# Kernel tuning notes

Hardware: AMD Instinct MI355X
Metric: run time of the kernel (lower is better)

## Reference

```python
import jax, jax.numpy as jnp
import numpy as np

B, T, D, H, C = 2048, 512, 1, 50, 2  # batch, seq_len, input_size, hidden_size, num_classes


def setup_inputs() -> dict:
    key = jax.random.key(0)
    ks = jax.random.split(key, 11)
    k = 1.0 / np.sqrt(H)  # torch default init bound
    u = lambda kk, shape: jax.random.uniform(kk, shape, jnp.float32, -k, k)
    return {
        "x": jax.random.normal(ks[0], (B, T, D), jnp.float32),
        "W_ih0": u(ks[1], (4 * H, D)),
        "W_hh0": u(ks[2], (4 * H, H)),
        "b_ih0": u(ks[3], (4 * H,)),
        "b_hh0": u(ks[4], (4 * H,)),
        "W_ih1": u(ks[5], (4 * H, H)),
        "W_hh1": u(ks[6], (4 * H, H)),
        "b_ih1": u(ks[7], (4 * H,)),
        "b_hh1": u(ks[8], (4 * H,)),
        "W_fc": u(ks[9], (C, H)),
        "b_fc": u(ks[10], (C,)),
    }


def _lstm_layer(x, Wih, Whh, bih, bhh):
    # x: [B, T, Din] -> hidden sequence [B, T, H]. PyTorch gate order: i, f, g, o.
    Bn = x.shape[0]
    Hn = Whh.shape[1]
    # precompute input contribution for all timesteps (one big GEMM)
    xg = jnp.einsum('btd,gd->btg', x, Wih) + bih + bhh  # [B, T, 4H]

    def step(carry, xg_t):
        h, c = carry
        g = xg_t + h @ Whh.T  # [B, 4H]
        i, f, gg, o = jnp.split(g, 4, axis=-1)
        i = jax.nn.sigmoid(i)
        f = jax.nn.sigmoid(f)
        gg = jnp.tanh(gg)
        o = jax.nn.sigmoid(o)
        c = f * c + i * gg
        h = o * jnp.tanh(c)
        return (h, c), h

    h0 = jnp.zeros((Bn, Hn), x.dtype)
    c0 = jnp.zeros((Bn, Hn), x.dtype)
    (_, _), hs = jax.lax.scan(step, (h0, c0), jnp.swapaxes(xg, 0, 1))  # hs: [T, B, H]
    return jnp.swapaxes(hs, 0, 1)


def reference(x, W_ih0, W_hh0, b_ih0, b_hh0, W_ih1, W_hh1, b_ih1, b_hh1, W_fc, b_fc):
    h1 = _lstm_layer(x, W_ih0, W_hh0, b_ih0, b_hh0)
    h2 = _lstm_layer(h1, W_ih1, W_hh1, b_ih1, b_hh1)
    # out[:, -1, :] @ W_fc.T + b_fc  (last-timestep hidden -> classifier)
    return h2[:, -1, :] @ W_fc.T + b_fc
```

## Files before the change

kernel.cpp:

```cpp
#include <hip/hip_runtime.h>

#define T_SEQ 512
#define HID   50
#define NB    8
#define BLK   832

typedef float v4f  __attribute__((ext_vector_type(4)));
typedef _Float16 f16;
typedef f16  f16x8 __attribute__((ext_vector_type(8)));


__device__ __forceinline__ f16x8 ldA0(const float* __restrict__ Whh0,
                                      const float* __restrict__ Wih0,
                                      const float* __restrict__ bih0,
                                      const float* __restrict__ bhh0,
                                      int m, int kb) {
    const int u = m >> 2, g = m & 3;
    f16x8 v;
    #pragma unroll
    for (int j = 0; j < 8; ++j) {
        const int k = kb + j;
        float f = 0.f;
        if (u < HID) {
            const int rho = g * HID + u;
            if (k < HID)      f = Whh0[rho * HID + k];
            else if (k == 62) f = Wih0[rho];
            else if (k == 63) f = bih0[rho] + bhh0[rho];
        }
        v[j] = (f16)f;
    }
    return v;
}

__device__ __forceinline__ f16x8 ldA1a(const float* __restrict__ Wih1,
                                       const float* __restrict__ bih1,
                                       const float* __restrict__ bhh1,
                                       int m, int kb) {
    const int u = m >> 2, g = m & 3;
    f16x8 v;
    #pragma unroll
    for (int j = 0; j < 8; ++j) {
        const int k = kb + j;
        float f = 0.f;
        if (u < HID) {
            const int rho = g * HID + u;
            if (k < HID)      f = Wih1[rho * HID + k];
            else if (k == 63) f = bih1[rho] + bhh1[rho];
        }
        v[j] = (f16)f;
    }
    return v;
}

__device__ __forceinline__ f16x8 ldA1b(const float* __restrict__ Whh1,
                                       int m, int kb) {
    const int u = m >> 2, g = m & 3;
    f16x8 v;
    #pragma unroll
    for (int j = 0; j < 8; ++j) {
        const int k = kb + j;
        float f = 0.f;
        if (u < HID && k < HID) f = Whh1[(g * HID + u) * HID + k];
        v[j] = (f16)f;
    }
    return v;
}

#define MFMA16(A, B, C) __builtin_amdgcn_mfma_f32_16x16x32_f16((A), (B), (C), 0, 0, 0)

__device__ __forceinline__ float lstm_epi(const v4f CC, float& cs) {
    const float e1 = __expf(-CC.x);
    const float e2 = __expf(-CC.y);
    const float e3 = __expf(-2.f * CC.z);
    const float e4 = __expf(-CC.w);
    const float d1 = 1.f + e1, d2 = 1.f + e2, d3 = 1.f + e3, d4 = 1.f + e4;
    const float p2 = d1 * d2, p3 = p2 * d3, p4 = p3 * d4;
    const float i4 = __builtin_amdgcn_rcpf(p4);
    const float go = i4 * p3;
    const float i3 = i4 * d4;
    const float r3 = i3 * p2;
    const float i2 = i3 * d3;
    const float gf = i2 * d1;
    const float gi = i2 * d2;
    const float gg = fmaf(2.f, r3, -1.f);
    cs = fmaf(gf, cs, gi * gg);
    const float th = fmaf(2.f, __builtin_amdgcn_rcpf(1.f + __expf(-2.f * cs)), -1.f);
    return go * th;
}

__global__ __launch_bounds__(BLK, 1)
void lstm2_mfma(const float* __restrict__ x,
                const float* __restrict__ Wih0,
                const float* __restrict__ Whh0,
                const float* __restrict__ bih0,
                const float* __restrict__ bhh0,
                const float* __restrict__ Wih1,
                const float* __restrict__ Whh1,
                const float* __restrict__ bih1,
                const float* __restrict__ bhh1,
                const float* __restrict__ Wfc,
                const float* __restrict__ bfc,
                float* __restrict__ out)
{
    __shared__ __align__(16) f16 BPH [8 * 64 * 8];
    __shared__ f16   xs16[NB][T_SEQ];
    __shared__ float hfin[HID][NB];

    const int tid  = threadIdx.x;
    const int w    = tid >> 6;
    const int lane = tid & 63;
    const int n16  = lane & 15;
    const int quad = lane >> 4;
    const int bb0  = blockIdx.x * NB;

    const float* xg = x + (long)bb0 * T_SEQ;

    for (int i = tid; i < 8 * 64 * 8; i += BLK) BPH[i] = (f16)0.f;
    for (int i = tid; i < NB * T_SEQ; i += BLK) {
        const int n = i >> 9, tt = i & (T_SEQ - 1);
        xs16[n][tt] = (f16)xg[n * T_SEQ + tt];
    }

    const int m   = w * 16 + n16;
    const int kb0 = quad * 8, kb1 = 32 + quad * 8;
    const f16x8 a0 = ldA0(Whh0, Wih0, bih0, bhh0, m, kb0);
    const f16x8 a1 = ldA0(Whh0, Wih0, bih0, bhh0, m, kb1);
    const f16x8 v0 = ldA1a(Wih1, bih1, bhh1, m, kb0);
    const f16x8 v1 = ldA1a(Wih1, bih1, bhh1, m, kb1);
    const f16x8 v2 = ldA1b(Whh1, m, kb0);
    const f16x8 v3 = ldA1b(Whh1, m, kb1);

    __syncthreads();
    if (tid < NB) {
        BPH[(1 * 64 + 48 + tid) * 8 + 7] = (f16)1.f;
        BPH[(1 * 64 + 56 + tid) * 8 + 7] = (f16)1.f;
        BPH[(3 * 64 + 48 + tid) * 8 + 7] = (f16)1.f;
        BPH[(3 * 64 + 56 + tid) * 8 + 7] = (f16)1.f;
        BPH[(3 * 64 + 48 + tid) * 8 + 6] = xs16[tid][0];
        BPH[(3 * 64 + 56 + tid) * 8 + 6] = xs16[tid][0];
    }
    __syncthreads();

    const int  u_    = w * 4 + quad;
    const bool isl0  = (n16 < 8);
    const bool valid = (u_ < HID);
    const int  wbase = (((u_ & 31) >> 3) * 16 + (n16 & 7)) * 8 + (u_ & 7) + (u_ >> 5) * 512;
    f16* const pwOdd  = &BPH[wbase + (isl0 ? 2 : 4) * 512];
    f16* const pwEven = &BPH[wbase + (isl0 ? 0 : 6) * 512];
    float cs = 0.f;
    const f16x8* BPF = (const f16x8*)BPH;
    const v4f CZ = {0.f, 0.f, 0.f, 0.f};

    {
        const f16x8 B0 = BPF[2 * 64 + lane];
        const f16x8 B1 = BPF[3 * 64 + lane];
        v4f D = MFMA16(a0, B0, CZ);  D = MFMA16(a1, B1, D);
        const float cs_sav = cs;
        const float hh = lstm_epi(D, cs);
        if (!isl0) cs = cs_sav;
        if (valid && isl0) { const f16 hv = (f16)hh; pwEven[0] = hv; pwEven[64] = hv; }
        if (w == 0 && lane < NB) {
            const f16 xv = xs16[lane][1];
            BPH[(1 * 64 + 48 + lane) * 8 + 6] = xv;
            BPH[(1 * 64 + 56 + lane) * 8 + 6] = xv;
        }
        __syncthreads();
    }

#define STEP(TA, TB, PW, XT, XS, DOX) {                                       \
        const f16x8 B0 = BPF[(TA)     * 64 + lane];                           \
        const f16x8 B1 = BPF[(TA + 1) * 64 + lane];                           \
        const f16x8 B2 = BPF[(TB)     * 64 + lane];                           \
        const f16x8 B3 = BPF[(TB + 1) * 64 + lane];                           \
        v4f D = MFMA16(a0, B0, CZ);  D = MFMA16(a1, B1, D);                   \
        v4f E = MFMA16(v0, B0, CZ);  E = MFMA16(v1, B1, E);                   \
        E = MFMA16(v2, B2, E);       E = MFMA16(v3, B3, E);                   \
        v4f CC;                                                               \
        CC.x = isl0 ? D.x : E.x;  CC.y = isl0 ? D.y : E.y;                    \
        CC.z = isl0 ? D.z : E.z;  CC.w = isl0 ? D.w : E.w;                    \
        const float hh = lstm_epi(CC, cs);                                    \
        if (valid) { const f16 hv = (f16)hh; (PW)[0] = hv; (PW)[64] = hv; }   \
        if ((DOX) && w == 0 && lane < NB) {                                   \
            const f16 xv = xs16[lane][(XS)];                                  \
            BPH[((XT) * 64 + 48 + lane) * 8 + 6] = xv;                        \
            BPH[((XT) * 64 + 56 + lane) * 8 + 6] = xv;                        \
        }                                                                     \
        __syncthreads(); }

    #pragma clang loop unroll(disable)
    for (int s = 1; s < 511; s += 2) {
        STEP(0, 6, pwOdd,  3, s + 1, true)
        STEP(2, 4, pwEven, 1, s + 2, true)
    }
    STEP(0, 6, pwOdd, 3, 0, false)

    {
        const f16x8 B0 = BPF[2 * 64 + lane];
        const f16x8 B1 = BPF[3 * 64 + lane];
        const f16x8 B2 = BPF[4 * 64 + lane];
        const f16x8 B3 = BPF[5 * 64 + lane];
        v4f E = MFMA16(v0, B0, CZ);  E = MFMA16(v1, B1, E);
        E = MFMA16(v2, B2, E);       E = MFMA16(v3, B3, E);
        const float hh = lstm_epi(E, cs);
        if (!isl0 && valid) hfin[u_][n16 & 7] = hh;
        __syncthreads();
    }

    if (tid < NB * 2) {
        const int nn = tid >> 1, c = tid & 1;
        float acc = bfc[c];
        #pragma unroll
        for (int u = 0; u < HID; ++u)
            acc = fmaf(Wfc[c * HID + u], hfin[u][nn], acc);
        out[(bb0 + nn) * 2 + c] = acc;
    }
}

extern "C" void kernel_launch(void* const* d_in, const int* in_sizes, int n_in,
                              void* d_out, int out_size, void* d_ws, size_t ws_size,
                              hipStream_t stream) {
    const float* x    = (const float*)d_in[0];
    const float* Wih0 = (const float*)d_in[1];
    const float* Whh0 = (const float*)d_in[2];
    const float* bih0 = (const float*)d_in[3];
    const float* bhh0 = (const float*)d_in[4];
    const float* Wih1 = (const float*)d_in[5];
    const float* Whh1 = (const float*)d_in[6];
    const float* bih1 = (const float*)d_in[7];
    const float* bhh1 = (const float*)d_in[8];
    const float* Wfc  = (const float*)d_in[9];
    const float* bfc  = (const float*)d_in[10];
    float* out = (float*)d_out;

    const int B = in_sizes[0] / T_SEQ;
    const int grid = B / NB;

    hipLaunchKernelGGL(lstm2_mfma, dim3(grid), dim3(BLK), 0, stream,
                       x, Wih0, Whh0, bih0, bhh0, Wih1, Whh1, bih1, bhh1,
                       Wfc, bfc, out);
}
```

Baseline: 327.3 us.

## Halve batch per block, double MFMA tiles per wave, fold log2e into weights

Each block now handles 4 sequences instead of 8 with 7 waves instead of 13. Each wave computes two 16-row gate tiles, and lanes pick their results from the two tiles so the 16 MFMA columns are used more fully. Launch bounds now allow up to 4 blocks per CU, with the aim of more concurrent blocks overlapping the per-step barriers and LDS latency. The log2(e) scaling, doubled for the g gate, is folded into the fp16 weights so the epilogue uses exp2 directly. The cost is twice the MFMA work per wave per step, more registers per thread, and slightly different fp16 rounding of the scaled weights.

```diff
diff --git a/kernel.cpp b/kernel.cpp
--- a/kernel.cpp
+++ b/kernel.cpp
@@ -2,13 +2,23 @@
 
 #define T_SEQ 512
 #define HID   50
-#define NB    8
-#define BLK   832
+#define NB    4
+#define BLK   448
 
 typedef float v4f  __attribute__((ext_vector_type(4)));
 typedef _Float16 f16;
 typedef f16  f16x8 __attribute__((ext_vector_type(8)));
 
+
+#define LOG2E 1.44269504f
+
+__device__ __forceinline__ float exp2g(float x) {
+#if __has_builtin(__builtin_amdgcn_exp2f)
+    return __builtin_amdgcn_exp2f(x);
+#else
+    return __builtin_exp2f(x);
+#endif
+}
 
 __device__ __forceinline__ f16x8 ldA0(const float* __restrict__ Whh0,
                                       const float* __restrict__ Wih0,
@@ -16,6 +26,7 @@
                                       const float* __restrict__ bhh0,
                                       int m, int kb) {
     const int u = m >> 2, g = m & 3;
+    const float sc = (g == 2) ? (2.f * LOG2E) : LOG2E;
     f16x8 v;
     #pragma unroll
     for (int j = 0; j < 8; ++j) {
@@ -27,7 +38,7 @@
             else if (k == 62) f = Wih0[rho];
             else if (k == 63) f = bih0[rho] + bhh0[rho];
         }
-        v[j] = (f16)f;
+        v[j] = (f16)(f * sc);
     }
     return v;
 }
@@ -37,6 +48,7 @@
                                        const float* __restrict__ bhh1,
                                        int m, int kb) {
     const int u = m >> 2, g = m & 3;
+    const float sc = (g == 2) ? (2.f * LOG2E) : LOG2E;
     f16x8 v;
     #pragma unroll
     for (int j = 0; j < 8; ++j) {
@@ -47,7 +59,7 @@
             if (k < HID)      f = Wih1[rho * HID + k];
             else if (k == 63) f = bih1[rho] + bhh1[rho];
         }
-        v[j] = (f16)f;
+        v[j] = (f16)(f * sc);
     }
     return v;
 }
@@ -55,13 +67,14 @@
 __device__ __forceinline__ f16x8 ldA1b(const float* __restrict__ Whh1,
                                        int m, int kb) {
     const int u = m >> 2, g = m & 3;
+    const float sc = (g == 2) ? (2.f * LOG2E) : LOG2E;
     f16x8 v;
     #pragma unroll
     for (int j = 0; j < 8; ++j) {
         const int k = kb + j;
         float f = 0.f;
         if (u < HID && k < HID) f = Whh1[(g * HID + u) * HID + k];
-        v[j] = (f16)f;
+        v[j] = (f16)(f * sc);
     }
     return v;
 }
@@ -69,10 +82,10 @@
 #define MFMA16(A, B, C) __builtin_amdgcn_mfma_f32_16x16x32_f16((A), (B), (C), 0, 0, 0)
 
 __device__ __forceinline__ float lstm_epi(const v4f CC, float& cs) {
-    const float e1 = __expf(-CC.x);
-    const float e2 = __expf(-CC.y);
-    const float e3 = __expf(-2.f * CC.z);
-    const float e4 = __expf(-CC.w);
+    const float e1 = exp2g(-CC.x);
+    const float e2 = exp2g(-CC.y);
+    const float e3 = exp2g(-CC.z);
+    const float e4 = exp2g(-CC.w);
     const float d1 = 1.f + e1, d2 = 1.f + e2, d3 = 1.f + e3, d4 = 1.f + e4;
     const float p2 = d1 * d2, p3 = p2 * d3, p4 = p3 * d4;
     const float i4 = __builtin_amdgcn_rcpf(p4);
@@ -84,11 +97,11 @@
     const float gi = i2 * d2;
     const float gg = fmaf(2.f, r3, -1.f);
     cs = fmaf(gf, cs, gi * gg);
-    const float th = fmaf(2.f, __builtin_amdgcn_rcpf(1.f + __expf(-2.f * cs)), -1.f);
+    const float th = fmaf(2.f, __builtin_amdgcn_rcpf(1.f + exp2g(-2.88539008f * cs)), -1.f);
     return go * th;
 }
 
-__global__ __launch_bounds__(BLK, 1)
+__global__ __launch_bounds__(BLK, 4)
 void lstm2_mfma(const float* __restrict__ x,
                 const float* __restrict__ Wih0,
                 const float* __restrict__ Whh0,
@@ -121,30 +134,37 @@
         xs16[n][tt] = (f16)xg[n * T_SEQ + tt];
     }
 
-    const int m   = w * 16 + n16;
+    const int mA  = (2 * w)     * 16 + n16;
+    const int mB  = (2 * w + 1) * 16 + n16;
     const int kb0 = quad * 8, kb1 = 32 + quad * 8;
-    const f16x8 a0 = ldA0(Whh0, Wih0, bih0, bhh0, m, kb0);
-    const f16x8 a1 = ldA0(Whh0, Wih0, bih0, bhh0, m, kb1);
-    const f16x8 v0 = ldA1a(Wih1, bih1, bhh1, m, kb0);
-    const f16x8 v1 = ldA1a(Wih1, bih1, bhh1, m, kb1);
-    const f16x8 v2 = ldA1b(Whh1, m, kb0);
-    const f16x8 v3 = ldA1b(Whh1, m, kb1);
+    const f16x8 a0A = ldA0(Whh0, Wih0, bih0, bhh0, mA, kb0);
+    const f16x8 a1A = ldA0(Whh0, Wih0, bih0, bhh0, mA, kb1);
+    const f16x8 a0B = ldA0(Whh0, Wih0, bih0, bhh0, mB, kb0);
+    const f16x8 a1B = ldA0(Whh0, Wih0, bih0, bhh0, mB, kb1);
+    const f16x8 v0A = ldA1a(Wih1, bih1, bhh1, mA, kb0);
+    const f16x8 v1A = ldA1a(Wih1, bih1, bhh1, mA, kb1);
+    const f16x8 v2A = ldA1b(Whh1, mA, kb0);
+    const f16x8 v3A = ldA1b(Whh1, mA, kb1);
+    const f16x8 v0B = ldA1a(Wih1, bih1, bhh1, mB, kb0);
+    const f16x8 v1B = ldA1a(Wih1, bih1, bhh1, mB, kb1);
+    const f16x8 v2B = ldA1b(Whh1, mB, kb0);
+    const f16x8 v3B = ldA1b(Whh1, mB, kb1);
 
     __syncthreads();
     if (tid < NB) {
         BPH[(1 * 64 + 48 + tid) * 8 + 7] = (f16)1.f;
-        BPH[(1 * 64 + 56 + tid) * 8 + 7] = (f16)1.f;
         BPH[(3 * 64 + 48 + tid) * 8 + 7] = (f16)1.f;
-        BPH[(3 * 64 + 56 + tid) * 8 + 7] = (f16)1.f;
         BPH[(3 * 64 + 48 + tid) * 8 + 6] = xs16[tid][0];
-        BPH[(3 * 64 + 56 + tid) * 8 + 6] = xs16[tid][0];
     }
     __syncthreads();
 
-    const int  u_    = w * 4 + quad;
+    const int  b_    = n16 & 3;
+    const bool uhb   = (n16 >> 2) & 1;
     const bool isl0  = (n16 < 8);
+    const int  u_    = 8 * w + (uhb ? 4 : 0) + quad;
     const bool valid = (u_ < HID);
-    const int  wbase = (((u_ & 31) >> 3) * 16 + (n16 & 7)) * 8 + (u_ & 7) + (u_ >> 5) * 512;
+    const int  rdl   = quad * 16 + b_;
+    const int  wbase = (((u_ & 31) >> 3) * 16 + b_) * 8 + (u_ & 7) + (u_ >> 5) * 512;
     f16* const pwOdd  = &BPH[wbase + (isl0 ? 2 : 4) * 512];
     f16* const pwEven = &BPH[wbase + (isl0 ? 0 : 6) * 512];
     float cs = 0.f;
@@ -152,39 +172,44 @@
     const v4f CZ = {0.f, 0.f, 0.f, 0.f};
 
     {
-        const f16x8 B0 = BPF[2 * 64 + lane];
-        const f16x8 B1 = BPF[3 * 64 + lane];
-        v4f D = MFMA16(a0, B0, CZ);  D = MFMA16(a1, B1, D);
+        const f16x8 B0 = BPF[2 * 64 + rdl];
+        const f16x8 B1 = BPF[3 * 64 + rdl];
+        v4f D0 = MFMA16(a0A, B0, CZ);  D0 = MFMA16(a1A, B1, D0);
+        v4f D1 = MFMA16(a0B, B0, CZ);  D1 = MFMA16(a1B, B1, D1);
+        v4f CC;
+        CC.x = uhb ? D1.x : D0.x;  CC.y = uhb ? D1.y : D0.y;
+        CC.z = uhb ? D1.z : D0.z;  CC.w = uhb ? D1.w : D0.w;
         const float cs_sav = cs;
-        const float hh = lstm_epi(D, cs);
+        const float hh = lstm_epi(CC, cs);
         if (!isl0) cs = cs_sav;
-        if (valid && isl0) { const f16 hv = (f16)hh; pwEven[0] = hv; pwEven[64] = hv; }
-        if (w == 0 && lane < NB) {
-            const f16 xv = xs16[lane][1];
-            BPH[(1 * 64 + 48 + lane) * 8 + 6] = xv;
-            BPH[(1 * 64 + 56 + lane) * 8 + 6] = xv;
-        }
+        if (valid && isl0) pwEven[0] = (f16)hh;
+        if (w == 0 && lane < NB)
+            BPH[(1 * 64 + 48 + lane) * 8 + 6] = xs16[lane][1];
         __syncthreads();
     }
 
 #define STEP(TA, TB, PW, XT, XS, DOX) {                                       \
-        const f16x8 B0 = BPF[(TA)     * 64 + lane];                           \
-        const f16x8 B1 = BPF[(TA + 1) * 64 + lane];                           \
-        const f16x8 B2 = BPF[(TB)     * 64 + lane];                           \
-        const f16x8 B3 = BPF[(TB + 1) * 64 + lane];                           \
-        v4f D = MFMA16(a0, B0, CZ);  D = MFMA16(a1, B1, D);                   \
-        v4f E = MFMA16(v0, B0, CZ);  E = MFMA16(v1, B1, E);                   \
-        E = MFMA16(v2, B2, E);       E = MFMA16(v3, B3, E);                   \
-        v4f CC;                                                               \
-        CC.x = isl0 ? D.x : E.x;  CC.y = isl0 ? D.y : E.y;                    \
-        CC.z = isl0 ? D.z : E.z;  CC.w = isl0 ? D.w : E.w;                    \
+        const f16x8 B0 = BPF[(TA)     * 64 + rdl];                            \
+        const f16x8 B1 = BPF[(TA + 1) * 64 + rdl];                            \
+        const f16x8 B2 = BPF[(TB)     * 64 + rdl];                            \
+        const f16x8 B3 = BPF[(TB + 1) * 64 + rdl];                            \
+        v4f D0 = MFMA16(a0A, B0, CZ);  D0 = MFMA16(a1A, B1, D0);              \
+        v4f D1 = MFMA16(a0B, B0, CZ);  D1 = MFMA16(a1B, B1, D1);              \
+        v4f E0 = MFMA16(v0A, B0, CZ);  E0 = MFMA16(v1A, B1, E0);              \
+        E0 = MFMA16(v2A, B2, E0);      E0 = MFMA16(v3A, B3, E0);              \
+        v4f E1 = MFMA16(v0B, B0, CZ);  E1 = MFMA16(v1B, B1, E1);              \
+        E1 = MFMA16(v2B, B2, E1);      E1 = MFMA16(v3B, B3, E1);              \
+        v4f Dd, Ee, CC;                                                       \
+        Dd.x = uhb ? D1.x : D0.x;  Dd.y = uhb ? D1.y : D0.y;                  \
+        Dd.z = uhb ? D1.z : D0.z;  Dd.w = uhb ? D1.w : D0.w;                  \
+        Ee.x = uhb ? E1.x : E0.x;  Ee.y = uhb ? E1.y : E0.y;                  \
+        Ee.z = uhb ? E1.z : E0.z;  Ee.w = uhb ? E1.w : E0.w;                  \
+        CC.x = isl0 ? Dd.x : Ee.x;  CC.y = isl0 ? Dd.y : Ee.y;                \
+        CC.z = isl0 ? Dd.z : Ee.z;  CC.w = isl0 ? Dd.w : Ee.w;                \
         const float hh = lstm_epi(CC, cs);                                    \
-        if (valid) { const f16 hv = (f16)hh; (PW)[0] = hv; (PW)[64] = hv; }   \
-        if ((DOX) && w == 0 && lane < NB) {                                   \
-            const f16 xv = xs16[lane][(XS)];                                  \
-            BPH[((XT) * 64 + 48 + lane) * 8 + 6] = xv;                        \
-            BPH[((XT) * 64 + 56 + lane) * 8 + 6] = xv;                        \
-        }                                                                     \
+        if (valid) (PW)[0] = (f16)hh;                                         \
+        if ((DOX) && w == 0 && lane < NB)                                     \
+            BPH[((XT) * 64 + 48 + lane) * 8 + 6] = xs16[lane][(XS)];          \
         __syncthreads(); }
 
     #pragma clang loop unroll(disable)
@@ -195,14 +220,19 @@
     STEP(0, 6, pwOdd, 3, 0, false)
 
     {
-        const f16x8 B0 = BPF[2 * 64 + lane];
-        const f16x8 B1 = BPF[3 * 64 + lane];
-        const f16x8 B2 = BPF[4 * 64 + lane];
-        const f16x8 B3 = BPF[5 * 64 + lane];
-        v4f E = MFMA16(v0, B0, CZ);  E = MFMA16(v1, B1, E);
-        E = MFMA16(v2, B2, E);       E = MFMA16(v3, B3, E);
-        const float hh = lstm_epi(E, cs);
-        if (!isl0 && valid) hfin[u_][n16 & 7] = hh;
+        const f16x8 B0 = BPF[2 * 64 + rdl];
+        const f16x8 B1 = BPF[3 * 64 + rdl];
+        const f16x8 B2 = BPF[4 * 64 + rdl];
+        const f16x8 B3 = BPF[5 * 64 + rdl];
+        v4f E0 = MFMA16(v0A, B0, CZ);  E0 = MFMA16(v1A, B1, E0);
+        E0 = MFMA16(v2A, B2, E0);      E0 = MFMA16(v3A, B3, E0);
+        v4f E1 = MFMA16(v0B, B0, CZ);  E1 = MFMA16(v1B, B1, E1);
+        E1 = MFMA16(v2B, B2, E1);      E1 = MFMA16(v3B, B3, E1);
+        v4f CC;
+        CC.x = uhb ? E1.x : E0.x;  CC.y = uhb ? E1.y : E0.y;
+        CC.z = uhb ? E1.z : E0.z;  CC.w = uhb ? E1.w : E0.w;
+        const float hh = lstm_epi(CC, cs);
+        if (!isl0 && valid) hfin[u_][b_] = hh;
         __syncthreads();
     }
 
```

After: 382.5 us. 1.17x slower.
